# Kernel optimization log

Hardware: AMD Instinct MI355X
Metric: run time of the kernel (lower is better)

Reference implementation:

```python
import jax, jax.numpy as jnp
import numpy as np

N = 200_000   # occupied voxels
G = 100
C = 128


def _kernel_maps():
    """Build Minkowski-style kernel maps for a 3x3x3 stride-1 sparse conv.
    Returns in_idx, out_idx of shape [27, N] (int32), padded with
    in=0 / out=N sentinel (row N of the scatter buffer is dropped)."""
    rng = np.random.default_rng(0)
    lin = rng.choice(G ** 3, size=N, replace=False)
    coords = np.stack(np.unravel_index(lin, (G, G, G)), axis=1).astype(np.int64)  # [N,3]
    lut = np.full(G ** 3, -1, np.int64)
    lut[lin] = np.arange(N)
    offs = np.array([[dx, dy, dz] for dx in (-1, 0, 1)
                     for dy in (-1, 0, 1) for dz in (-1, 0, 1)], np.int64)
    in_idx = np.zeros((27, N), np.int32)
    out_idx = np.full((27, N), N, np.int32)
    for k, off in enumerate(offs):
        nb = coords + off
        valid = np.all((nb >= 0) & (nb < G), axis=1)
        nb_lin = (nb[:, 0] * G + nb[:, 1]) * G + nb[:, 2]
        j = np.where(valid, lut[np.clip(nb_lin, 0, G ** 3 - 1)], -1)
        sel = np.nonzero(j >= 0)[0]
        m = sel.size
        in_idx[k, :m] = j[sel].astype(np.int32)
        out_idx[k, :m] = sel.astype(np.int32)
    return jnp.asarray(in_idx), jnp.asarray(out_idx)


def setup_inputs() -> dict:
    key = jax.random.key(0)
    ks = jax.random.split(key, 8)
    in_idx, out_idx = _kernel_maps()
    s = 0.02
    return {
        "x_F": jax.random.normal(ks[0], (N, C), jnp.float32),
        "xg_F": jax.random.normal(ks[1], (N, C), jnp.float32),
        "W0": jax.random.normal(ks[2], (27, C, C), jnp.float32) * s,
        "b0": jax.random.normal(ks[3], (C,), jnp.float32) * s,
        "W1": jax.random.normal(ks[4], (27, C, C), jnp.float32) * s,
        "b1": jax.random.normal(ks[5], (C,), jnp.float32) * s,
        "W2": jax.random.normal(ks[6], (27, 2 * C, C), jnp.float32) * s,
        "b2": jax.random.normal(ks[7], (C,), jnp.float32) * s,
        "in_idx": in_idx,
        "out_idx": out_idx,
    }


def _sparse_conv(feat, W, b, in_idx, out_idx):
    # gather-matmul-scatter over the 27 kernel offsets
    n = feat.shape[0]
    cout = W.shape[-1]
    out = jnp.zeros((n + 1, cout), feat.dtype)  # row n is the pad sink
    for k in range(W.shape[0]):
        out = out.at[out_idx[k]].add(feat[in_idx[k]] @ W[k])
    return out[:n] + b


def reference(x_F, xg_F, W0, b0, W1, b1, W2, b2, in_idx, out_idx):
    h = _sparse_conv(xg_F, W0, b0, in_idx, out_idx)          # conv0
    h = jax.nn.relu(_sparse_conv(h, W1, b1, in_idx, out_idx))  # relu(conv1(.))
    cat = jnp.concatenate([x_F, h], axis=1)                   # [N, 2C]
    return _sparse_conv(cat, W2, b2, in_idx, out_idx)         # conv2
```

## Files before the change

### kernel.cpp

```cpp
#include <hip/hip_runtime.h>

#define NV   200000
#define CC   128
#define KOFF 27

typedef unsigned short u16;
typedef __attribute__((ext_vector_type(4))) float f32x4;
typedef __attribute__((ext_vector_type(8))) short bf16x8;

__device__ __forceinline__ u16 f2bf(float f) {
    unsigned u = __float_as_uint(f);
    u += 0x7fffu + ((u >> 16) & 1u);
    return (u16)(u >> 16);
}

#define GLOAD16(gp, lp)                                                        \
    __builtin_amdgcn_global_load_lds(                                          \
        (const __attribute__((address_space(1))) void*)(gp),                   \
        (__attribute__((address_space(3))) void*)(lp), 16, 0, 0)

__global__ void gmap_kernel(const int* __restrict__ iin,
                            const int* __restrict__ iout,
                            int* __restrict__ gmap) {
    int t = blockIdx.x * 256 + threadIdx.x;
    if (t >= KOFF * NV) return;
    int o = iout[t];
    if (o < NV) {
        int k = t / NV;
        gmap[k * NV + o] = iin[t];
    }
}

__global__ void cvt_kernel(const float* __restrict__ src,
                           u16* __restrict__ dst, int n4) {
    int i = blockIdx.x * 256 + threadIdx.x;
    if (i >= n4) return;
    float4 v = ((const float4*)src)[i];
    ushort4 o;
    o.x = f2bf(v.x); o.y = f2bf(v.y); o.z = f2bf(v.z); o.w = f2bf(v.w);
    ((ushort4*)dst)[i] = o;
}

__global__ void packw_kernel(const float* __restrict__ W,
                             u16* __restrict__ Wp, int cin, int total) {
    int t = blockIdx.x * 256 + threadIdx.x;
    if (t >= total) return;
    int j  = t & 7;
    int l  = (t >> 3) & 63;
    int cf = (t >> 9) & 7;
    int sk = t >> 12;
    int nks = cin >> 5;
    int k  = sk / nks;
    int ks = sk - k * nks;
    int kpos = ks * 32 + (l >> 4) * 8 + j;
    int col  = cf * 16 + (l & 15);
    Wp[t] = f2bf(W[((size_t)k * cin + kpos) * CC + col]);
}

template <int NKS, int ACT, int OUT16>
__global__ __launch_bounds__(256, 2)
void conv_kernel(const u16* __restrict__ f0, const u16* __restrict__ f1,
                 const u16* __restrict__ Wp, const float* __restrict__ bias,
                 const int* __restrict__ gmap, const u16* __restrict__ zrow,
                 float* __restrict__ out32, u16* __restrict__ out16) {
    constexpr int NSTEP = KOFF * NKS;

    __shared__ u16 Ab[2][512 * 8];
    __shared__ u16 Bb[2][8][64][8];

    const int tid = threadIdx.x;
    const int l   = tid & 63;
    const int w   = tid >> 6;
    const int wr  = w >> 1, wc = w & 1;
    const int r0  = blockIdx.x * 128;

    const int qA  = (l & 3) ^ ((l >> 3) & 3);
    const int rA0 = 32 * w + (l >> 2);
    const int rA1 = rA0 + 16;

    float bcol[4];
#pragma unroll
    for (int c = 0; c < 4; ++c) bcol[c] = bias[wc * 64 + c * 16 + (l & 15)];

    f32x4 acc[4][4] = {};

    int gA, gB;
    auto loadGmap = [&](int s) {
        int k = s / NKS;
        int ra = r0 + rA0, rb = r0 + rA1;
        gA = (ra < NV) ? gmap[k * NV + ra] : -1;
        gB = (rb < NV) ? gmap[k * NV + rb] : -1;
    };

    auto stage = [&](int s, int buf) {
        int k = s / NKS, ks = s - k * NKS;
        const u16* base;
        int slice;
        if constexpr (NKS == 8) {
            base  = (ks < 4) ? f0 : f1;
            slice = (ks & 3) * 32;
        } else {
            base  = f0;
            slice = ks * 32;
        }
        const u16* sA0 = (gA >= 0) ? base + (size_t)gA * CC + slice + qA * 8
                                   : zrow + qA * 8;
        const u16* sA1 = (gB >= 0) ? base + (size_t)gB * CC + slice + qA * 8
                                   : zrow + qA * 8;
        GLOAD16(sA0, &Ab[buf][(2 * w) * 64 * 8]);
        GLOAD16(sA1, &Ab[buf][(2 * w + 1) * 64 * 8]);
        const u16* wsrc = Wp + (((size_t)(k * NKS + ks) * 8 + 2 * w) * 512) + l * 8;
        GLOAD16(wsrc,       &Bb[buf][2 * w][0][0]);
        GLOAD16(wsrc + 512, &Bb[buf][2 * w + 1][0][0]);
    };

    auto compute = [&](int buf) {
        bf16x8 a[4], b[4];
        const int q = l >> 4;
#pragma unroll
        for (int rf = 0; rf < 4; ++rf) {
            int rl = wr * 64 + rf * 16 + (l & 15);
            int ci = rl * 4 + (q ^ ((rl >> 1) & 3));
            a[rf] = *(const bf16x8*)&Ab[buf][ci * 8];
        }
#pragma unroll
        for (int c = 0; c < 4; ++c)
            b[c] = *(const bf16x8*)&Bb[buf][wc * 4 + c][l][0];
#pragma unroll
        for (int rf = 0; rf < 4; ++rf)
#pragma unroll
            for (int c = 0; c < 4; ++c)
                acc[rf][c] = __builtin_amdgcn_mfma_f32_16x16x32_bf16(
                    a[rf], b[c], acc[rf][c], 0, 0, 0);
    };

    loadGmap(0);
    stage(0, 0);
    loadGmap(1);
    __syncthreads();

    int cur = 0;
    for (int s = 0; s < NSTEP; ++s) {
        if (s + 1 < NSTEP) {
            stage(s + 1, cur ^ 1);
            if (s + 2 < NSTEP) loadGmap(s + 2);
        }
        compute(cur);
        __syncthreads();
        cur ^= 1;
    }

#pragma unroll
    for (int rf = 0; rf < 4; ++rf) {
        int rbase = r0 + wr * 64 + rf * 16 + (l >> 4) * 4;
#pragma unroll
        for (int i = 0; i < 4; ++i) {
            int row = rbase + i;
            if (row < NV) {
#pragma unroll
                for (int c = 0; c < 4; ++c) {
                    float v = acc[rf][c][i] + bcol[c];
                    if constexpr (ACT) v = fmaxf(v, 0.f);
                    int col = wc * 64 + c * 16 + (l & 15);
                    if constexpr (OUT16) out16[(size_t)row * CC + col] = f2bf(v);
                    else                 out32[(size_t)row * CC + col] = v;
                }
            }
        }
    }
}

extern "C" void kernel_launch(void* const* d_in, const int* in_sizes, int n_in,
                              void* d_out, int out_size, void* d_ws, size_t ws_size,
                              hipStream_t stream) {
    (void)in_sizes; (void)n_in; (void)out_size; (void)ws_size;
    const float* xF  = (const float*)d_in[0];
    const float* xgF = (const float*)d_in[1];
    const float* W0  = (const float*)d_in[2];
    const float* b0  = (const float*)d_in[3];
    const float* W1  = (const float*)d_in[4];
    const float* b1  = (const float*)d_in[5];
    const float* W2  = (const float*)d_in[6];
    const float* b2  = (const float*)d_in[7];
    const int* iin   = (const int*)d_in[8];
    const int* iout  = (const int*)d_in[9];
    float* out = (float*)d_out;
    char* ws = (char*)d_ws;

    size_t off = 0;
    int* gmap  = (int*)(ws + off);  off += (size_t)KOFF * NV * 4;
    u16* zrow  = (u16*)(ws + off);  off += 256;
    u16* F0    = (u16*)(ws + off);  off += (size_t)NV * CC * 2;
    u16* F1    = (u16*)(ws + off);  off += (size_t)NV * CC * 2;
    u16* F2    = (u16*)(ws + off);  off += (size_t)NV * CC * 2;
    u16* WP0   = (u16*)(ws + off);  off += (size_t)KOFF * 128 * 128 * 2;
    u16* WP1   = (u16*)(ws + off);  off += (size_t)KOFF * 128 * 128 * 2;
    u16* WP2   = (u16*)(ws + off);  off += (size_t)KOFF * 256 * 128 * 2;

    (void)hipMemsetAsync(gmap, 0xFF, (size_t)KOFF * NV * 4, stream);
    (void)hipMemsetAsync(zrow, 0, 256, stream);

    gmap_kernel<<<(KOFF * NV + 255) / 256, 256, 0, stream>>>(iin, iout, gmap);
    cvt_kernel<<<(NV * CC / 4 + 255) / 256, 256, 0, stream>>>(xgF, F0, NV * CC / 4);
    cvt_kernel<<<(NV * CC / 4 + 255) / 256, 256, 0, stream>>>(xF,  F2, NV * CC / 4);
    packw_kernel<<<(KOFF * 128 * 128 + 255) / 256, 256, 0, stream>>>(W0, WP0, 128, KOFF * 128 * 128);
    packw_kernel<<<(KOFF * 128 * 128 + 255) / 256, 256, 0, stream>>>(W1, WP1, 128, KOFF * 128 * 128);
    packw_kernel<<<(KOFF * 256 * 128 + 255) / 256, 256, 0, stream>>>(W2, WP2, 256, KOFF * 256 * 128);

    const int NB = (NV + 127) / 128;
    conv_kernel<4, 0, 1><<<NB, 256, 0, stream>>>(F0, F0, WP0, b0, gmap, zrow, nullptr, F1);
    conv_kernel<4, 1, 1><<<NB, 256, 0, stream>>>(F1, F1, WP1, b1, gmap, zrow, nullptr, F0);
    conv_kernel<8, 0, 0><<<NB, 256, 0, stream>>>(F2, F0, WP2, b2, gmap, zrow, out, nullptr);
}
```

Measured before the change: 774.2 us.

## Load weight fragments directly into registers and raise occupancy bound

Removes the LDS staging buffer for the weight tiles. Each wave now loads its four B fragments straight from global memory into double-buffered registers, and the main loop is unrolled by two to alternate between the two register sets. Launch bounds go from 2 to 4 blocks per CU, since LDS use is halved. This cuts LDS traffic and shared-memory footprint. In exchange, global and L2 weight loads are duplicated across waves, and the tighter register budget risks spills.

```diff
diff --git a/kernel.cpp b/kernel.cpp
--- a/kernel.cpp
+++ b/kernel.cpp
@@ -58,7 +58,7 @@
 }
 
 template <int NKS, int ACT, int OUT16>
-__global__ __launch_bounds__(256, 2)
+__global__ __launch_bounds__(256, 4)
 void conv_kernel(const u16* __restrict__ f0, const u16* __restrict__ f1,
                  const u16* __restrict__ Wp, const float* __restrict__ bias,
                  const int* __restrict__ gmap, const u16* __restrict__ zrow,
@@ -66,7 +66,6 @@
     constexpr int NSTEP = KOFF * NKS;
 
     __shared__ u16 Ab[2][512 * 8];
-    __shared__ u16 Bb[2][8][64][8];
 
     const int tid = threadIdx.x;
     const int l   = tid & 63;
@@ -109,13 +108,18 @@
                                    : zrow + qA * 8;
         GLOAD16(sA0, &Ab[buf][(2 * w) * 64 * 8]);
         GLOAD16(sA1, &Ab[buf][(2 * w + 1) * 64 * 8]);
-        const u16* wsrc = Wp + (((size_t)(k * NKS + ks) * 8 + 2 * w) * 512) + l * 8;
-        GLOAD16(wsrc,       &Bb[buf][2 * w][0][0]);
-        GLOAD16(wsrc + 512, &Bb[buf][2 * w + 1][0][0]);
-    };
-
-    auto compute = [&](int buf) {
-        bf16x8 a[4], b[4];
+    };
+
+    auto loadB = [&](int s, bf16x8 (&bfr)[4]) {
+        int k = s / NKS, ks = s - k * NKS;
+        const u16* wsrc = Wp + (((size_t)(k * NKS + ks) * 8 + wc * 4) * 512) + l * 8;
+#pragma unroll
+        for (int c = 0; c < 4; ++c)
+            bfr[c] = *(const bf16x8*)(wsrc + (size_t)c * 512);
+    };
+
+    auto compute = [&](int buf, const bf16x8 (&bfr)[4]) {
+        bf16x8 a[4];
         const int q = l >> 4;
 #pragma unroll
         for (int rf = 0; rf < 4; ++rf) {
@@ -124,30 +128,41 @@
             a[rf] = *(const bf16x8*)&Ab[buf][ci * 8];
         }
 #pragma unroll
-        for (int c = 0; c < 4; ++c)
-            b[c] = *(const bf16x8*)&Bb[buf][wc * 4 + c][l][0];
-#pragma unroll
         for (int rf = 0; rf < 4; ++rf)
 #pragma unroll
             for (int c = 0; c < 4; ++c)
                 acc[rf][c] = __builtin_amdgcn_mfma_f32_16x16x32_bf16(
-                    a[rf], b[c], acc[rf][c], 0, 0, 0);
-    };
+                    a[rf], bfr[c], acc[rf][c], 0, 0, 0);
+    };
+
+    bf16x8 bA[4], bB[4];
 
     loadGmap(0);
     stage(0, 0);
+    loadB(0, bA);
     loadGmap(1);
     __syncthreads();
 
     int cur = 0;
-    for (int s = 0; s < NSTEP; ++s) {
-        if (s + 1 < NSTEP) {
+    for (int s = 0; s < NSTEP; s += 2) {
+        {
             stage(s + 1, cur ^ 1);
+            loadB(s + 1, bB);
             if (s + 2 < NSTEP) loadGmap(s + 2);
-        }
-        compute(cur);
-        __syncthreads();
-        cur ^= 1;
+            compute(cur, bA);
+            __syncthreads();
+            cur ^= 1;
+        }
+        {
+            if (s + 2 < NSTEP) {
+                stage(s + 2, cur ^ 1);
+                loadB(s + 2, bA);
+                if (s + 3 < NSTEP) loadGmap(s + 3);
+            }
+            compute(cur, bB);
+            __syncthreads();
+            cur ^= 1;
+        }
     }
 
 #pragma unroll
```

New measurement: 795.0 us. 1.03x slower.

## Split sparse conv into compact per-offset GEMMs plus gather-reduce pass

Applied to the files above, without the earlier changes.

Replaces the output-stationary gather-GEMM over all 27 offsets, which ran MFMA on zero-padded rows for missing neighbours, with two phases. Phase A runs a GEMM per kernel offset over only the valid compacted pairs and writes bf16 partial products into a temp buffer, with each offset capped at a fixed capacity. Phase B uses a reverse map to gather and sum the 27 partials per output row, then adds bias and ReLU. Output channels are split into two halves to bound temp size. This cuts wasted MFMA work on empty neighbours, but adds a round trip to the temp buffer, rounds intermediates to bf16, and relies on a hardcoded per-offset capacity (CAPK) that must fit the input distribution.

```diff
diff --git a/kernel.cpp b/kernel.cpp
--- a/kernel.cpp
+++ b/kernel.cpp
@@ -3,6 +3,8 @@
 #define NV   200000
 #define CC   128
 #define KOFF 27
+#define CAPK 42000
+#define TROWS (26 * CAPK + NV)
 
 typedef unsigned short u16;
 typedef __attribute__((ext_vector_type(4))) float f32x4;
@@ -13,21 +15,23 @@
     u += 0x7fffu + ((u >> 16) & 1u);
     return (u16)(u >> 16);
 }
+__device__ __forceinline__ size_t tbase(int k) {
+    return (size_t)k * CAPK + (k > 13 ? (NV - CAPK) : 0);
+}
 
 #define GLOAD16(gp, lp)                                                        \
     __builtin_amdgcn_global_load_lds(                                          \
         (const __attribute__((address_space(1))) void*)(gp),                   \
         (__attribute__((address_space(3))) void*)(lp), 16, 0, 0)
 
-__global__ void gmap_kernel(const int* __restrict__ iin,
-                            const int* __restrict__ iout,
-                            int* __restrict__ gmap) {
+__global__ void rmap_kernel(const int* __restrict__ iout,
+                            int* __restrict__ rmap) {
     int t = blockIdx.x * 256 + threadIdx.x;
     if (t >= KOFF * NV) return;
     int o = iout[t];
     if (o < NV) {
         int k = t / NV;
-        gmap[k * NV + o] = iin[t];
+        rmap[(size_t)k * NV + o] = t - k * NV;
     }
 }
 
@@ -57,43 +61,31 @@
     Wp[t] = f2bf(W[((size_t)k * cin + kpos) * CC + col]);
 }
 
-template <int NKS, int ACT, int OUT16>
-__global__ __launch_bounds__(256, 2)
-void conv_kernel(const u16* __restrict__ f0, const u16* __restrict__ f1,
-                 const u16* __restrict__ Wp, const float* __restrict__ bias,
-                 const int* __restrict__ gmap, const u16* __restrict__ zrow,
-                 float* __restrict__ out32, u16* __restrict__ out16) {
-    constexpr int NSTEP = KOFF * NKS;
+template <int NKS>
+__global__ __launch_bounds__(256, 4)
+void convA_kernel(const u16* __restrict__ f0, const u16* __restrict__ f1,
+                  const u16* __restrict__ Wp, const int* __restrict__ iidx,
+                  const int* __restrict__ oidx, u16* __restrict__ T, int hc) {
+    const int k  = blockIdx.y;
+    const int r0 = blockIdx.x * 128;
+    if (oidx[(size_t)k * NV + r0] >= NV) return;
 
     __shared__ u16 Ab[2][512 * 8];
-    __shared__ u16 Bb[2][8][64][8];
+    __shared__ u16 Bb[2][4][64][8];
 
     const int tid = threadIdx.x;
     const int l   = tid & 63;
     const int w   = tid >> 6;
-    const int wr  = w >> 1, wc = w & 1;
-    const int r0  = blockIdx.x * 128;
 
     const int qA  = (l & 3) ^ ((l >> 3) & 3);
-    const int rA0 = 32 * w + (l >> 2);
-    const int rA1 = rA0 + 16;
-
-    float bcol[4];
-#pragma unroll
-    for (int c = 0; c < 4; ++c) bcol[c] = bias[wc * 64 + c * 16 + (l & 15)];
-
-    f32x4 acc[4][4] = {};
-
-    int gA, gB;
-    auto loadGmap = [&](int s) {
-        int k = s / NKS;
-        int ra = r0 + rA0, rb = r0 + rA1;
-        gA = (ra < NV) ? gmap[k * NV + ra] : -1;
-        gB = (rb < NV) ? gmap[k * NV + rb] : -1;
-    };
-
-    auto stage = [&](int s, int buf) {
-        int k = s / NKS, ks = s - k * NKS;
+    int ra = r0 + 32 * w + (l >> 2); if (ra >= NV) ra = NV - 1;
+    int rb = ra + 16;                if (rb >= NV) rb = NV - 1;
+    const int gA = iidx[(size_t)k * NV + ra];
+    const int gB = iidx[(size_t)k * NV + rb];
+
+    f32x4 acc[2][4] = {};
+
+    auto stage = [&](int ks, int buf) {
         const u16* base;
         int slice;
         if constexpr (NKS == 8) {
@@ -103,68 +95,124 @@
             base  = f0;
             slice = ks * 32;
         }
-        const u16* sA0 = (gA >= 0) ? base + (size_t)gA * CC + slice + qA * 8
-                                   : zrow + qA * 8;
-        const u16* sA1 = (gB >= 0) ? base + (size_t)gB * CC + slice + qA * 8
-                                   : zrow + qA * 8;
-        GLOAD16(sA0, &Ab[buf][(2 * w) * 64 * 8]);
-        GLOAD16(sA1, &Ab[buf][(2 * w + 1) * 64 * 8]);
-        const u16* wsrc = Wp + (((size_t)(k * NKS + ks) * 8 + 2 * w) * 512) + l * 8;
-        GLOAD16(wsrc,       &Bb[buf][2 * w][0][0]);
-        GLOAD16(wsrc + 512, &Bb[buf][2 * w + 1][0][0]);
+        GLOAD16(base + (size_t)gA * CC + slice + qA * 8, &Ab[buf][(2 * w) * 512]);
+        GLOAD16(base + (size_t)gB * CC + slice + qA * 8, &Ab[buf][(2 * w + 1) * 512]);
+        const u16* wsrc = Wp + ((size_t)(k * NKS + ks) * 8 + hc * 4 + w) * 512 + l * 8;
+        GLOAD16(wsrc, &Bb[buf][w][0][0]);
     };
 
     auto compute = [&](int buf) {
-        bf16x8 a[4], b[4];
+        bf16x8 a[2], b[4];
         const int q = l >> 4;
 #pragma unroll
-        for (int rf = 0; rf < 4; ++rf) {
-            int rl = wr * 64 + rf * 16 + (l & 15);
+        for (int rf = 0; rf < 2; ++rf) {
+            int rl = w * 32 + rf * 16 + (l & 15);
             int ci = rl * 4 + (q ^ ((rl >> 1) & 3));
             a[rf] = *(const bf16x8*)&Ab[buf][ci * 8];
         }
 #pragma unroll
         for (int c = 0; c < 4; ++c)
-            b[c] = *(const bf16x8*)&Bb[buf][wc * 4 + c][l][0];
-#pragma unroll
-        for (int rf = 0; rf < 4; ++rf)
+            b[c] = *(const bf16x8*)&Bb[buf][c][l][0];
+#pragma unroll
+        for (int rf = 0; rf < 2; ++rf)
 #pragma unroll
             for (int c = 0; c < 4; ++c)
                 acc[rf][c] = __builtin_amdgcn_mfma_f32_16x16x32_bf16(
                     a[rf], b[c], acc[rf][c], 0, 0, 0);
     };
 
-    loadGmap(0);
     stage(0, 0);
-    loadGmap(1);
     __syncthreads();
-
-    int cur = 0;
-    for (int s = 0; s < NSTEP; ++s) {
-        if (s + 1 < NSTEP) {
-            stage(s + 1, cur ^ 1);
-            if (s + 2 < NSTEP) loadGmap(s + 2);
-        }
-        compute(cur);
+#pragma unroll
+    for (int s = 0; s < NKS; ++s) {
+        if (s + 1 < NKS) stage(s + 1, (s + 1) & 1);
+        compute(s & 1);
         __syncthreads();
-        cur ^= 1;
-    }
-
-#pragma unroll
-    for (int rf = 0; rf < 4; ++rf) {
-        int rbase = r0 + wr * 64 + rf * 16 + (l >> 4) * 4;
+    }
+
+    const int   cap = (k == 13) ? NV : CAPK;
+    const size_t tb = tbase(k);
+#pragma unroll
+    for (int rf = 0; rf < 2; ++rf) {
+        int rbase = r0 + w * 32 + rf * 16 + (l >> 4) * 4;
 #pragma unroll
         for (int i = 0; i < 4; ++i) {
-            int row = rbase + i;
-            if (row < NV) {
-#pragma unroll
-                for (int c = 0; c < 4; ++c) {
-                    float v = acc[rf][c][i] + bcol[c];
+            int trow = rbase + i;
+            if (trow < cap) {
+                u16* dst = T + (tb + trow) * 64 + (l & 15);
+#pragma unroll
+                for (int c = 0; c < 4; ++c)
+                    dst[c * 16] = f2bf(acc[rf][c][i]);
+            }
+        }
+    }
+}
+
+template <int ACT, int OUT16>
+__global__ __launch_bounds__(256, 4)
+void convB_kernel(const u16* __restrict__ T, const int* __restrict__ rmap,
+                  const float* __restrict__ bias,
+                  float* __restrict__ out32, u16* __restrict__ out16, int hc) {
+    __shared__ int   sm[KOFF * 256];
+    __shared__ float sb[64];
+    const int r0  = blockIdx.x * 256;
+    const int tid = threadIdx.x;
+
+    for (int j = tid; j < KOFF * 256; j += 256) {
+        int k = j >> 8, rr = j & 255;
+        int o = r0 + rr;
+        sm[j] = (o < NV) ? rmap[(size_t)k * NV + o] : -1;
+    }
+    if (tid < 64) sb[tid] = bias[hc * 64 + tid];
+    __syncthreads();
+
+    float acc[64];
+#pragma unroll
+    for (int j = 0; j < 64; ++j) acc[j] = sb[j];
+
+    for (int k = 0; k < KOFF; ++k) {
+        int t = sm[k * 256 + tid];
+        if (t < 0) continue;
+        const u16* p = T + (tbase(k) + (size_t)t) * 64;
+#pragma unroll
+        for (int c = 0; c < 8; ++c) {
+            bf16x8 v = *(const bf16x8*)(p + c * 8);
+#pragma unroll
+            for (int j = 0; j < 8; ++j) {
+                unsigned uu = ((unsigned)(u16)v[j]) << 16;
+                acc[c * 8 + j] += __uint_as_float(uu);
+            }
+        }
+    }
+
+    const int r = r0 + tid;
+    if (r < NV) {
+        if constexpr (OUT16) {
+            u16* d = out16 + (size_t)r * CC + hc * 64;
+#pragma unroll
+            for (int c = 0; c < 8; ++c) {
+                bf16x8 pk;
+#pragma unroll
+                for (int j = 0; j < 8; ++j) {
+                    float v = acc[c * 8 + j];
                     if constexpr (ACT) v = fmaxf(v, 0.f);
-                    int col = wc * 64 + c * 16 + (l & 15);
-                    if constexpr (OUT16) out16[(size_t)row * CC + col] = f2bf(v);
-                    else                 out32[(size_t)row * CC + col] = v;
+                    pk[j] = (short)f2bf(v);
                 }
+                *(bf16x8*)(d + c * 8) = pk;
+            }
+        } else {
+            float* d = out32 + (size_t)r * CC + hc * 64;
+#pragma unroll
+            for (int c = 0; c < 16; ++c) {
+                float4 pk;
+                float v0 = acc[c * 4 + 0], v1 = acc[c * 4 + 1];
+                float v2 = acc[c * 4 + 2], v3 = acc[c * 4 + 3];
+                if constexpr (ACT) {
+                    v0 = fmaxf(v0, 0.f); v1 = fmaxf(v1, 0.f);
+                    v2 = fmaxf(v2, 0.f); v3 = fmaxf(v3, 0.f);
+                }
+                pk.x = v0; pk.y = v1; pk.z = v2; pk.w = v3;
+                *(float4*)(d + c * 4) = pk;
             }
         }
     }
@@ -188,27 +236,37 @@
     char* ws = (char*)d_ws;
 
     size_t off = 0;
-    int* gmap  = (int*)(ws + off);  off += (size_t)KOFF * NV * 4;
-    u16* zrow  = (u16*)(ws + off);  off += 256;
+    int* rmap  = (int*)(ws + off);  off += (size_t)KOFF * NV * 4;
     u16* F0    = (u16*)(ws + off);  off += (size_t)NV * CC * 2;
     u16* F1    = (u16*)(ws + off);  off += (size_t)NV * CC * 2;
     u16* F2    = (u16*)(ws + off);  off += (size_t)NV * CC * 2;
     u16* WP0   = (u16*)(ws + off);  off += (size_t)KOFF * 128 * 128 * 2;
     u16* WP1   = (u16*)(ws + off);  off += (size_t)KOFF * 128 * 128 * 2;
     u16* WP2   = (u16*)(ws + off);  off += (size_t)KOFF * 256 * 128 * 2;
-
-    (void)hipMemsetAsync(gmap, 0xFF, (size_t)KOFF * NV * 4, stream);
-    (void)hipMemsetAsync(zrow, 0, 256, stream);
-
-    gmap_kernel<<<(KOFF * NV + 255) / 256, 256, 0, stream>>>(iin, iout, gmap);
+    u16* T     = (u16*)(ws + off);  off += (size_t)TROWS * 64 * 2;
+
+    (void)hipMemsetAsync(rmap, 0xFF, (size_t)KOFF * NV * 4, stream);
+
+    rmap_kernel<<<(KOFF * NV + 255) / 256, 256, 0, stream>>>(iout, rmap);
     cvt_kernel<<<(NV * CC / 4 + 255) / 256, 256, 0, stream>>>(xgF, F0, NV * CC / 4);
     cvt_kernel<<<(NV * CC / 4 + 255) / 256, 256, 0, stream>>>(xF,  F2, NV * CC / 4);
     packw_kernel<<<(KOFF * 128 * 128 + 255) / 256, 256, 0, stream>>>(W0, WP0, 128, KOFF * 128 * 128);
     packw_kernel<<<(KOFF * 128 * 128 + 255) / 256, 256, 0, stream>>>(W1, WP1, 128, KOFF * 128 * 128);
     packw_kernel<<<(KOFF * 256 * 128 + 255) / 256, 256, 0, stream>>>(W2, WP2, 256, KOFF * 256 * 128);
 
-    const int NB = (NV + 127) / 128;
-    conv_kernel<4, 0, 1><<<NB, 256, 0, stream>>>(F0, F0, WP0, b0, gmap, zrow, nullptr, F1);
-    conv_kernel<4, 1, 1><<<NB, 256, 0, stream>>>(F1, F1, WP1, b1, gmap, zrow, nullptr, F0);
-    conv_kernel<8, 0, 0><<<NB, 256, 0, stream>>>(F2, F0, WP2, b2, gmap, zrow, out, nullptr);
-}
+    const dim3 gA((NV + 127) / 128, KOFF);
+    const int  gB = (NV + 255) / 256;
+
+    for (int hc = 0; hc < 2; ++hc) {
+        convA_kernel<4><<<gA, 256, 0, stream>>>(F0, F0, WP0, iin, iout, T, hc);
+        convB_kernel<0, 1><<<gB, 256, 0, stream>>>(T, rmap, b0, nullptr, F1, hc);
+    }
+    for (int hc = 0; hc < 2; ++hc) {
+        convA_kernel<4><<<gA, 256, 0, stream>>>(F1, F1, WP1, iin, iout, T, hc);
+        convB_kernel<1, 1><<<gB, 256, 0, stream>>>(T, rmap, b1, nullptr, F0, hc);
+    }
+    for (int hc = 0; hc < 2; ++hc) {
+        convA_kernel<8><<<gA, 256, 0, stream>>>(F2, F0, WP2, iin, iout, T, hc);
+        convB_kernel<0, 0><<<gB, 256, 0, stream>>>(T, rmap, b2, out, nullptr, hc);
+    }
+}
```

Result: slower. 1.158 ms (+49.6%).

## Deepen conv pipeline to 4 LDS stages and preload gather indices into LDS

Applied to the files above, without the earlier changes.

Replaces the double-buffered gather/weight staging with a 4-buffer ring that issues loads three steps ahead, waiting on explicit vmcnt counts and a raw s_barrier rather than a full __syncthreads after every step. The block's gmap entries for all 27 offsets are preloaded into LDS once at kernel start, so per-step index lookups become LDS reads instead of dependent global loads. MFMA sections are wrapped in s_setprio. The costs are more LDS per block, which may limit residency under the 2-blocks launch bound, and hand-counted vmcnt waits that must stay in step with the number of loads issued per stage. The gmap buffer is padded and memset so the tail block's index preload stays in bounds.

```diff
diff --git a/kernel.cpp b/kernel.cpp
--- a/kernel.cpp
+++ b/kernel.cpp
@@ -18,6 +18,16 @@
     __builtin_amdgcn_global_load_lds(                                          \
         (const __attribute__((address_space(1))) void*)(gp),                   \
         (__attribute__((address_space(3))) void*)(lp), 16, 0, 0)
+
+#define WAITV8()                                                               \
+    do { asm volatile("s_waitcnt vmcnt(8)" ::: "memory");                      \
+         __builtin_amdgcn_sched_barrier(0); } while (0)
+#define WAITV4()                                                               \
+    do { asm volatile("s_waitcnt vmcnt(4)" ::: "memory");                      \
+         __builtin_amdgcn_sched_barrier(0); } while (0)
+#define WAITV0()                                                               \
+    do { asm volatile("s_waitcnt vmcnt(0)" ::: "memory");                      \
+         __builtin_amdgcn_sched_barrier(0); } while (0)
 
 __global__ void gmap_kernel(const int* __restrict__ iin,
                             const int* __restrict__ iout,
@@ -65,8 +75,9 @@
                  float* __restrict__ out32, u16* __restrict__ out16) {
     constexpr int NSTEP = KOFF * NKS;
 
-    __shared__ u16 Ab[2][512 * 8];
-    __shared__ u16 Bb[2][8][64][8];
+    __shared__ u16 Ab[4][4096];
+    __shared__ u16 Bb[4][8][64][8];
+    __shared__ int gmT[4096];
 
     const int tid = threadIdx.x;
     const int l   = tid & 63;
@@ -84,16 +95,24 @@
 
     f32x4 acc[4][4] = {};
 
-    int gA, gB;
-    auto loadGmap = [&](int s) {
+#pragma unroll
+    for (int p = 0; p < 4; ++p) {
+        int c = p * 256 + w * 64 + l;
+        int k = c >> 5; if (k > 26) k = 26;
+        const int* src = gmap + (size_t)k * NV + r0 + ((c * 4) & 127);
+        GLOAD16(src, (char*)gmT + (size_t)(p * 256 + w * 64) * 16);
+    }
+    WAITV0();
+    __builtin_amdgcn_s_barrier();
+
+    auto idxrd = [&](int s, int& g0, int& g1) {
         int k = s / NKS;
-        int ra = r0 + rA0, rb = r0 + rA1;
-        gA = (ra < NV) ? gmap[k * NV + ra] : -1;
-        gB = (rb < NV) ? gmap[k * NV + rb] : -1;
+        g0 = gmT[k * 128 + rA0];
+        g1 = gmT[k * 128 + rA1];
     };
 
-    auto stage = [&](int s, int buf) {
-        int k = s / NKS, ks = s - k * NKS;
+    auto stage = [&](int s, int buf, int g0, int g1) {
+        int ks = s % NKS;
         const u16* base;
         int slice;
         if constexpr (NKS == 8) {
@@ -103,12 +122,13 @@
             base  = f0;
             slice = ks * 32;
         }
-        const u16* sA0 = (gA >= 0) ? base + (size_t)gA * CC + slice + qA * 8
+        const u16* sA0 = (g0 >= 0) ? base + (size_t)g0 * CC + slice + qA * 8
                                    : zrow + qA * 8;
-        const u16* sA1 = (gB >= 0) ? base + (size_t)gB * CC + slice + qA * 8
+        const u16* sA1 = (g1 >= 0) ? base + (size_t)g1 * CC + slice + qA * 8
                                    : zrow + qA * 8;
-        GLOAD16(sA0, &Ab[buf][(2 * w) * 64 * 8]);
-        GLOAD16(sA1, &Ab[buf][(2 * w + 1) * 64 * 8]);
+        GLOAD16(sA0, &Ab[buf][(2 * w) * 512]);
+        GLOAD16(sA1, &Ab[buf][(2 * w + 1) * 512]);
+        int k = s / NKS;
         const u16* wsrc = Wp + (((size_t)(k * NKS + ks) * 8 + 2 * w) * 512) + l * 8;
         GLOAD16(wsrc,       &Bb[buf][2 * w][0][0]);
         GLOAD16(wsrc + 512, &Bb[buf][2 * w + 1][0][0]);
@@ -126,28 +146,35 @@
 #pragma unroll
         for (int c = 0; c < 4; ++c)
             b[c] = *(const bf16x8*)&Bb[buf][wc * 4 + c][l][0];
+        __builtin_amdgcn_s_setprio(1);
 #pragma unroll
         for (int rf = 0; rf < 4; ++rf)
 #pragma unroll
             for (int c = 0; c < 4; ++c)
                 acc[rf][c] = __builtin_amdgcn_mfma_f32_16x16x32_bf16(
                     a[rf], b[c], acc[rf][c], 0, 0, 0);
+        __builtin_amdgcn_s_setprio(0);
     };
 
-    loadGmap(0);
-    stage(0, 0);
-    loadGmap(1);
-    __syncthreads();
-
-    int cur = 0;
-    for (int s = 0; s < NSTEP; ++s) {
-        if (s + 1 < NSTEP) {
-            stage(s + 1, cur ^ 1);
-            if (s + 2 < NSTEP) loadGmap(s + 2);
-        }
-        compute(cur);
-        __syncthreads();
-        cur ^= 1;
+    {
+        int t0, t1;
+        idxrd(0, t0, t1); stage(0, 0, t0, t1);
+        idxrd(1, t0, t1); stage(1, 1, t0, t1);
+        idxrd(2, t0, t1); stage(2, 2, t0, t1);
+    }
+    int gC0, gC1, gN0, gN1;
+    idxrd(3, gC0, gC1);
+    idxrd(4, gN0, gN1);
+
+    for (int t = 0; t < NSTEP; ++t) {
+        if (t + 2 < NSTEP)      { WAITV8(); }
+        else if (t + 1 < NSTEP) { WAITV4(); }
+        else                    { WAITV0(); }
+        __builtin_amdgcn_s_barrier();
+        if (t + 3 < NSTEP) stage(t + 3, (t + 3) & 3, gC0, gC1);
+        gC0 = gN0; gC1 = gN1;
+        if (t + 5 < NSTEP) idxrd(t + 5, gN0, gN1);
+        compute(t & 3);
     }
 
 #pragma unroll
@@ -188,7 +215,7 @@
     char* ws = (char*)d_ws;
 
     size_t off = 0;
-    int* gmap  = (int*)(ws + off);  off += (size_t)KOFF * NV * 4;
+    int* gmap  = (int*)(ws + off);  off += ((size_t)KOFF * NV + 512) * 4;
     u16* zrow  = (u16*)(ws + off);  off += 256;
     u16* F0    = (u16*)(ws + off);  off += (size_t)NV * CC * 2;
     u16* F1    = (u16*)(ws + off);  off += (size_t)NV * CC * 2;
@@ -197,7 +224,7 @@
     u16* WP1   = (u16*)(ws + off);  off += (size_t)KOFF * 128 * 128 * 2;
     u16* WP2   = (u16*)(ws + off);  off += (size_t)KOFF * 256 * 128 * 2;
 
-    (void)hipMemsetAsync(gmap, 0xFF, (size_t)KOFF * NV * 4, stream);
+    (void)hipMemsetAsync(gmap, 0xFF, ((size_t)KOFF * NV + 512) * 4, stream);
     (void)hipMemsetAsync(zrow, 0, 256, stream);
 
     gmap_kernel<<<(KOFF * NV + 255) / 256, 256, 0, stream>>>(iin, iout, gmap);
```

After: 1.314 ms. +69.7%, slower.
